# Kernel optimization log

Measured on AMD Instinct MI355X. Metric: run time of the kernel, lower is better.

## Reference

```python
import jax, jax.numpy as jnp
import numpy as np

WINDOW = 128
BACKWARD = 1
FORWARD = 0

def look_around(x, pad_value):
    # x: [b, windows, window_size, ...]; pad window axis and gather shifted windows
    w = x.shape[1]
    pads = [(0, 0), (BACKWARD, FORWARD)] + [(0, 0)] * (x.ndim - 2)
    p = jnp.pad(x, pads, constant_values=pad_value)
    return jnp.concatenate([p[:, i:i + w] for i in range(BACKWARD + FORWARD + 1)], axis=2)

def setup_inputs() -> dict:
    key = jax.random.key(0)
    ks = jax.random.split(key, 5)
    shp = (2, 16, 4096, 64)
    names = ['q', 'k', 'q_rot', 'k_rot', 'v']
    inp = {n: jax.random.normal(ks[i], shp, dtype=jnp.float32) for i, n in enumerate(names)}
    inp['states'] = 0
    inp['inferring_states'] = 0
    return inp

def reference(q, k, q_rot, k_rot, v, states, inferring_states):
    shape = q.shape
    merge = lambda t: t.reshape(-1, t.shape[-2], t.shape[-1])
    q, k, q_rot, k_rot, v = map(merge, (q, k, q_rot, k_rot, v))
    b, t, e = q.shape
    windows = t // WINDOW
    ticker = jnp.arange(t, dtype=q.dtype)[None, :]
    b_t = ticker.reshape(1, windows, WINDOW)
    bucket = lambda x: x.reshape(b, windows, WINDOW, e)
    bq, bk, bq_rot, bk_rot, bv = map(bucket, (q, k, q_rot, k_rot, v))
    bk = look_around(bk, 0.0)
    bk_rot = look_around(bk_rot, 0.0)
    bv = look_around(bv, 0.0)
    bq_t = b_t
    bq_k = look_around(b_t, -1.0)
    scale = e ** (-0.5)
    dots = jnp.einsum('bwie,bwje->bwij', bq, bk) * scale
    dots_rot = jnp.einsum('bwie,bwje->bwij', bq_rot, bk_rot) * scale
    mask_value = -jnp.finfo(dots.dtype).max
    causal_mask = bq_t[:, :, :, None] < bq_k[:, :, None, :]
    pad_mask = bq_k[:, :, None, :] == -1
    mask = causal_mask | pad_mask
    dots = jnp.where(mask, mask_value, dots)
    dots_rot = jnp.where(mask, mask_value, dots_rot)
    attn = jax.nn.softmax(dots + dots_rot, axis=-1)
    out = jnp.einsum('bwij,bwje->bwie', attn, bv)
    return out.reshape(shape)
```

## Files before the change

### kernel.cpp

```cpp
#include <hip/hip_runtime.h>
#include <stdint.h>

#define T 4096
#define E 64
#define NBH 32
#define W 4
#define LDK 136
#define CHUNK_KK (128*LDK)
#define CHUNK_VT (64*LDK)
#define BUF_ELEMS (CHUNK_KK + CHUNK_VT)
#define SMEM_BYTES (2*BUF_ELEMS*2)

typedef __attribute__((ext_vector_type(8))) short short8;
typedef __attribute__((ext_vector_type(4))) short short4v;
typedef __attribute__((ext_vector_type(4))) float f32x4;

__device__ __forceinline__ short f2bf(float x) {
  unsigned u = __float_as_uint(x);
  u += 0x7fffu + ((u >> 16) & 1u);
  return (short)(u >> 16);
}

struct ChunkStage { float4 sk[8]; float sv[16]; };

__device__ __forceinline__ void chunk_issue(ChunkStage& st,
    const float* __restrict__ k, const float* __restrict__ kr,
    const float* __restrict__ v, size_t rowbase, int tid, int wid, int lane) {
#pragma unroll
  for (int m = 0; m < 2; ++m) {
    const float* src = m ? kr : k;
#pragma unroll
    for (int it = 0; it < 4; ++it) {
      int idx = it * 512 + tid;
      st.sk[m * 4 + it] = *(const float4*)(src + (rowbase + (idx >> 4)) * E + (idx & 15) * 4);
    }
  }
  const float* vp = v + (rowbase + wid * 16) * E + lane;
#pragma unroll
  for (int i = 0; i < 16; ++i) st.sv[i] = vp[(size_t)i * E];
}

__device__ __forceinline__ void chunk_commit(const ChunkStage& st,
    short* __restrict__ KK, short* __restrict__ Vt, int tid, int wid, int lane) {
#pragma unroll
  for (int m = 0; m < 2; ++m) {
#pragma unroll
    for (int it = 0; it < 4; ++it) {
      int idx = it * 512 + tid;
      float4 f = st.sk[m * 4 + it];
      short4v h = { f2bf(f.x), f2bf(f.y), f2bf(f.z), f2bf(f.w) };
      *(short4v*)(KK + (idx >> 4) * LDK + m * 64 + (idx & 15) * 4) = h;
    }
  }
#pragma unroll
  for (int rq = 0; rq < 4; ++rq) {
    short4v h = { f2bf(st.sv[rq*4+0]), f2bf(st.sv[rq*4+1]),
                  f2bf(st.sv[rq*4+2]), f2bf(st.sv[rq*4+3]) };
    *(short4v*)(Vt + lane * LDK + wid * 16 + rq * 4) = h;
  }
}

__device__ __forceinline__ void q_issue(float4* sq,
    const float* __restrict__ q, const float* __restrict__ qr,
    size_t rbase, int w, int wid, int li, int lg) {
  const size_t qrow = rbase + (size_t)w * 128 + wid * 16 + li;
#pragma unroll
  for (int kt = 0; kt < 4; ++kt) {
    const float* sp = (kt < 2 ? q : qr) + qrow * E + (kt & 1) * 32 + lg * 8;
    sq[kt * 2 + 0] = *(const float4*)sp;
    sq[kt * 2 + 1] = *(const float4*)(sp + 4);
  }
}

__device__ __forceinline__ void q_commit(const float4* sq, short8* aF) {
#pragma unroll
  for (int kt = 0; kt < 4; ++kt) {
    float4 f0 = sq[kt * 2], f1 = sq[kt * 2 + 1];
    short8 a;
    a[0]=f2bf(f0.x*0.125f); a[1]=f2bf(f0.y*0.125f); a[2]=f2bf(f0.z*0.125f); a[3]=f2bf(f0.w*0.125f);
    a[4]=f2bf(f1.x*0.125f); a[5]=f2bf(f1.y*0.125f); a[6]=f2bf(f1.z*0.125f); a[7]=f2bf(f1.w*0.125f);
    aF[kt] = a;
  }
}

__global__ __launch_bounds__(512, 2)
void la_attn(const float* __restrict__ qg, const float* __restrict__ kg,
             const float* __restrict__ qrg, const float* __restrict__ krg,
             const float* __restrict__ vg, float* __restrict__ outg) {
  extern __shared__ short smem[];

  const int strip = blockIdx.x, bh = blockIdx.y;
  const int w0 = strip * W;
  const int tid = threadIdx.x;
  const int wid = tid >> 6, lane = tid & 63;
  const int li = lane & 15, lg = lane >> 4;
  const size_t rbase = (size_t)bh * T;
  const int rowb = wid * 16 + lg * 4;

  short8 aF[4];

  {
    ChunkStage s1, s0;
    float4 sq[8];
    if (w0 > 0) chunk_issue(s1, kg, krg, vg, rbase + (size_t)(w0 - 1) * 128, tid, wid, lane);
    chunk_issue(s0, kg, krg, vg, rbase + (size_t)w0 * 128, tid, wid, lane);
    q_issue(sq, qg, qrg, rbase, w0, wid, li, lg);
    if (w0 > 0) chunk_commit(s1, smem + BUF_ELEMS, smem + BUF_ELEMS + CHUNK_KK, tid, wid, lane);
    chunk_commit(s0, smem, smem + CHUNK_KK, tid, wid, lane);
    q_commit(sq, aF);
  }
  __syncthreads();

  for (int j = 0; j < W; ++j) {
    short* bufb = smem + ((j + 1) & 1) * BUF_ELEMS;
    short* bufc = smem + (j & 1) * BUF_ELEMS;
    short* KKback = bufb;       short* Vtback = bufb + CHUNK_KK;
    short* KKcur  = bufc;       short* Vtcur  = bufc + CHUNK_KK;
    const bool have_next = (j + 1 < W);
    const bool skipback = (w0 == 0 && j == 0);

    ChunkStage st;
    float4 sq[8];
    if (have_next) {
      chunk_issue(st, kg, krg, vg, rbase + (size_t)(w0 + j + 1) * 128, tid, wid, lane);
      q_issue(sq, qg, qrg, rbase, w0 + j + 1, wid, li, lg);
    }

    f32x4 S[16];
    if (!skipback) {
#pragma unroll
      for (int ct = 0; ct < 8; ++ct) {
        f32x4 acc = {0.f, 0.f, 0.f, 0.f};
        const short* kb = KKback + (ct * 16 + li) * LDK + lg * 8;
#pragma unroll
        for (int kt = 0; kt < 4; ++kt)
          acc = __builtin_amdgcn_mfma_f32_16x16x32_bf16(aF[kt], *(const short8*)(kb + kt * 32), acc, 0, 0, 0);
        S[ct] = acc;
      }
    } else {
#pragma unroll
      for (int ct = 0; ct < 8; ++ct) S[ct] = f32x4{-1e30f, -1e30f, -1e30f, -1e30f};
    }
#pragma unroll
    for (int ct = 0; ct < 8; ++ct) {
      f32x4 acc = {0.f, 0.f, 0.f, 0.f};
      const short* kb = KKcur + (ct * 16 + li) * LDK + lg * 8;
#pragma unroll
      for (int kt = 0; kt < 4; ++kt)
        acc = __builtin_amdgcn_mfma_f32_16x16x32_bf16(aF[kt], *(const short8*)(kb + kt * 32), acc, 0, 0, 0);
      S[8 + ct] = acc;
    }

    float linv[4];
#pragma unroll
    for (int r = 0; r < 4; ++r) {
      const int qi = rowb + r;
#pragma unroll
      for (int ct = 8; ct < 16; ++ct) {
        int jj = (ct - 8) * 16 + li;
        if (jj > qi) S[ct][r] = -1e30f;
      }
      float mx = -1e30f;
#pragma unroll
      for (int ct = 0; ct < 16; ++ct) mx = fmaxf(mx, S[ct][r]);
      mx = fmaxf(mx, __shfl_xor(mx, 1));
      mx = fmaxf(mx, __shfl_xor(mx, 2));
      mx = fmaxf(mx, __shfl_xor(mx, 4));
      mx = fmaxf(mx, __shfl_xor(mx, 8));
      float sm = 0.f;
#pragma unroll
      for (int ct = 0; ct < 16; ++ct) {
        float e = __expf(S[ct][r] - mx);
        S[ct][r] = e;
        sm += e;
      }
      sm += __shfl_xor(sm, 1);
      sm += __shfl_xor(sm, 2);
      sm += __shfl_xor(sm, 4);
      sm += __shfl_xor(sm, 8);
      linv[r] = 1.f / sm;
    }
    __syncthreads();

    short* pw = KKback + wid * 16 * LDK;
    f32x4 O[4] = {{0,0,0,0},{0,0,0,0},{0,0,0,0},{0,0,0,0}};
#pragma unroll
    for (int h = 0; h < 2; ++h) {
      if (h == 0 && skipback) continue;
      const short* Vth = h ? Vtcur : Vtback;
#pragma unroll
      for (int cc = 0; cc < 8; ++cc)
#pragma unroll
        for (int r = 0; r < 4; ++r)
          pw[(lg * 4 + r) * LDK + cc * 16 + li] = f2bf(S[h * 8 + cc][r]);
#pragma unroll
      for (int kt = 0; kt < 4; ++kt) {
        short8 aP = *(const short8*)(pw + li * LDK + kt * 32 + lg * 8);
#pragma unroll
        for (int nt = 0; nt < 4; ++nt) {
          short8 b = *(const short8*)(Vth + (nt * 16 + li) * LDK + kt * 32 + lg * 8);
          O[nt] = __builtin_amdgcn_mfma_f32_16x16x32_bf16(aP, b, O[nt], 0, 0, 0);
        }
      }
    }

    float* op = outg + (rbase + (size_t)(w0 + j) * 128 + rowb) * E;
#pragma unroll
    for (int r = 0; r < 4; ++r)
#pragma unroll
      for (int nt = 0; nt < 4; ++nt)
        op[(size_t)r * E + nt * 16 + li] = O[nt][r] * linv[r];

    __syncthreads();

    if (have_next) {
      chunk_commit(st, KKback, Vtback, tid, wid, lane);
      q_commit(sq, aF);
    }
    __syncthreads();
  }
}

extern "C" void kernel_launch(void* const* d_in, const int* in_sizes, int n_in,
                              void* d_out, int out_size, void* d_ws, size_t ws_size,
                              hipStream_t stream) {
  const float* q  = (const float*)d_in[0];
  const float* k  = (const float*)d_in[1];
  const float* qr = (const float*)d_in[2];
  const float* kr = (const float*)d_in[3];
  const float* v  = (const float*)d_in[4];
  float* out = (float*)d_out;
  la_attn<<<dim3(8, NBH), 512, SMEM_BYTES, stream>>>(q, k, qr, kr, v, out);
}
```

Measured before the change: 206.2 us.

## Split window softmax into online two-chunk pass and pipeline chunk loads two ahead

```diff
diff --git a/kernel.cpp b/kernel.cpp
--- a/kernel.cpp
+++ b/kernel.cpp
@@ -9,7 +9,8 @@
 #define CHUNK_KK (128*LDK)
 #define CHUNK_VT (64*LDK)
 #define BUF_ELEMS (CHUNK_KK + CHUNK_VT)
-#define SMEM_BYTES (2*BUF_ELEMS*2)
+#define PW_ELEMS (16*LDK)
+#define SMEM_BYTES ((2*BUF_ELEMS + 8*PW_ELEMS)*2)
 
 typedef __attribute__((ext_vector_type(8))) short short8;
 typedef __attribute__((ext_vector_type(4))) short short4v;
@@ -19,6 +20,12 @@
   unsigned u = __float_as_uint(x);
   u += 0x7fffu + ((u >> 16) & 1u);
   return (short)(u >> 16);
+}
+
+__device__ __forceinline__ void block_sync_lds() {
+  asm volatile("s_waitcnt lgkmcnt(0)" ::: "memory");
+  __builtin_amdgcn_s_barrier();
+  asm volatile("" ::: "memory");
 }
 
 struct ChunkStage { float4 sk[8]; float sv[16]; };
@@ -97,37 +104,40 @@
   const size_t rbase = (size_t)bh * T;
   const int rowb = wid * 16 + lg * 4;
 
+  short* PW = smem + 2 * BUF_ELEMS + wid * PW_ELEMS;
+  const int pxor_w = lg << 4;
+  const int pxor_r = (li >> 2) << 4;
+
   short8 aF[4];
+  ChunkStage st;
 
   {
-    ChunkStage s1, s0;
+    ChunkStage sm1, s0;
     float4 sq[8];
-    if (w0 > 0) chunk_issue(s1, kg, krg, vg, rbase + (size_t)(w0 - 1) * 128, tid, wid, lane);
+    if (w0 > 0) chunk_issue(sm1, kg, krg, vg, rbase + (size_t)(w0 - 1) * 128, tid, wid, lane);
     chunk_issue(s0, kg, krg, vg, rbase + (size_t)w0 * 128, tid, wid, lane);
     q_issue(sq, qg, qrg, rbase, w0, wid, li, lg);
-    if (w0 > 0) chunk_commit(s1, smem + BUF_ELEMS, smem + BUF_ELEMS + CHUNK_KK, tid, wid, lane);
+    if (w0 > 0) chunk_commit(sm1, smem + BUF_ELEMS, smem + BUF_ELEMS + CHUNK_KK, tid, wid, lane);
     chunk_commit(s0, smem, smem + CHUNK_KK, tid, wid, lane);
     q_commit(sq, aF);
-  }
-  __syncthreads();
+    chunk_issue(st, kg, krg, vg, rbase + (size_t)(w0 + 1) * 128, tid, wid, lane);
+  }
+  block_sync_lds();
 
   for (int j = 0; j < W; ++j) {
     short* bufb = smem + ((j + 1) & 1) * BUF_ELEMS;
     short* bufc = smem + (j & 1) * BUF_ELEMS;
     short* KKback = bufb;       short* Vtback = bufb + CHUNK_KK;
     short* KKcur  = bufc;       short* Vtcur  = bufc + CHUNK_KK;
-    const bool have_next = (j + 1 < W);
     const bool skipback = (w0 == 0 && j == 0);
 
-    ChunkStage st;
-    float4 sq[8];
-    if (have_next) {
-      chunk_issue(st, kg, krg, vg, rbase + (size_t)(w0 + j + 1) * 128, tid, wid, lane);
-      q_issue(sq, qg, qrg, rbase, w0 + j + 1, wid, li, lg);
-    }
-
-    f32x4 S[16];
+    float m[4], l[4];
+    f32x4 O[4] = {{0,0,0,0},{0,0,0,0},{0,0,0,0},{0,0,0,0}};
+#pragma unroll
+    for (int r = 0; r < 4; ++r) { m[r] = -1e30f; l[r] = 0.f; }
+
     if (!skipback) {
+      f32x4 S[8];
 #pragma unroll
       for (int ct = 0; ct < 8; ++ct) {
         f32x4 acc = {0.f, 0.f, 0.f, 0.f};
@@ -137,87 +147,124 @@
           acc = __builtin_amdgcn_mfma_f32_16x16x32_bf16(aF[kt], *(const short8*)(kb + kt * 32), acc, 0, 0, 0);
         S[ct] = acc;
       }
-    } else {
-#pragma unroll
-      for (int ct = 0; ct < 8; ++ct) S[ct] = f32x4{-1e30f, -1e30f, -1e30f, -1e30f};
-    }
-#pragma unroll
-    for (int ct = 0; ct < 8; ++ct) {
-      f32x4 acc = {0.f, 0.f, 0.f, 0.f};
-      const short* kb = KKcur + (ct * 16 + li) * LDK + lg * 8;
-#pragma unroll
-      for (int kt = 0; kt < 4; ++kt)
-        acc = __builtin_amdgcn_mfma_f32_16x16x32_bf16(aF[kt], *(const short8*)(kb + kt * 32), acc, 0, 0, 0);
-      S[8 + ct] = acc;
-    }
-
-    float linv[4];
+#pragma unroll
+      for (int r = 0; r < 4; ++r) {
+        float mx = S[0][r];
+#pragma unroll
+        for (int ct = 1; ct < 8; ++ct) mx = fmaxf(mx, S[ct][r]);
+        mx = fmaxf(mx, __shfl_xor(mx, 1));
+        mx = fmaxf(mx, __shfl_xor(mx, 2));
+        mx = fmaxf(mx, __shfl_xor(mx, 4));
+        mx = fmaxf(mx, __shfl_xor(mx, 8));
+        float sm = 0.f;
+#pragma unroll
+        for (int ct = 0; ct < 8; ++ct) {
+          float e = __expf(S[ct][r] - mx);
+          S[ct][r] = e;
+          sm += e;
+        }
+        sm += __shfl_xor(sm, 1);
+        sm += __shfl_xor(sm, 2);
+        sm += __shfl_xor(sm, 4);
+        sm += __shfl_xor(sm, 8);
+        m[r] = mx; l[r] = sm;
+      }
+#pragma unroll
+      for (int cc = 0; cc < 8; ++cc)
+#pragma unroll
+        for (int r = 0; r < 4; ++r)
+          PW[(lg * 4 + r) * LDK + ((cc * 16 + li) ^ pxor_w)] = f2bf(S[cc][r]);
+#pragma unroll
+      for (int kt = 0; kt < 4; ++kt) {
+        short8 aP = *(const short8*)(PW + li * LDK + ((kt * 32 + lg * 8) ^ pxor_r));
+#pragma unroll
+        for (int nt = 0; nt < 4; ++nt) {
+          short8 b = *(const short8*)(Vtback + (nt * 16 + li) * LDK + kt * 32 + lg * 8);
+          O[nt] = __builtin_amdgcn_mfma_f32_16x16x32_bf16(aP, b, O[nt], 0, 0, 0);
+        }
+      }
+    }
+
+    block_sync_lds();
+
+    const bool have_next = (j + 1 < W);
+    if (have_next) chunk_commit(st, KKback, Vtback, tid, wid, lane);
+    float4 sq[8];
+    if (j + 2 < W) chunk_issue(st, kg, krg, vg, rbase + (size_t)(w0 + j + 2) * 128, tid, wid, lane);
+    if (have_next) q_issue(sq, qg, qrg, rbase, w0 + j + 1, wid, li, lg);
+    asm volatile("" ::: "memory");
+
+    {
+      f32x4 S[8];
+#pragma unroll
+      for (int ct = 0; ct < 8; ++ct) {
+        f32x4 acc = {0.f, 0.f, 0.f, 0.f};
+        const short* kb = KKcur + (ct * 16 + li) * LDK + lg * 8;
+#pragma unroll
+        for (int kt = 0; kt < 4; ++kt)
+          acc = __builtin_amdgcn_mfma_f32_16x16x32_bf16(aF[kt], *(const short8*)(kb + kt * 32), acc, 0, 0, 0);
+        S[ct] = acc;
+      }
+#pragma unroll
+      for (int r = 0; r < 4; ++r) {
+        const int qi = rowb + r;
+#pragma unroll
+        for (int ct = 0; ct < 8; ++ct) {
+          int jj = ct * 16 + li;
+          if (jj > qi) S[ct][r] = -1e30f;
+        }
+        float mx = S[0][r];
+#pragma unroll
+        for (int ct = 1; ct < 8; ++ct) mx = fmaxf(mx, S[ct][r]);
+        mx = fmaxf(mx, __shfl_xor(mx, 1));
+        mx = fmaxf(mx, __shfl_xor(mx, 2));
+        mx = fmaxf(mx, __shfl_xor(mx, 4));
+        mx = fmaxf(mx, __shfl_xor(mx, 8));
+        float mn = fmaxf(m[r], mx);
+        float f = __expf(m[r] - mn);
+        float sm = 0.f;
+#pragma unroll
+        for (int ct = 0; ct < 8; ++ct) {
+          float e = __expf(S[ct][r] - mn);
+          S[ct][r] = e;
+          sm += e;
+        }
+        sm += __shfl_xor(sm, 1);
+        sm += __shfl_xor(sm, 2);
+        sm += __shfl_xor(sm, 4);
+        sm += __shfl_xor(sm, 8);
+        l[r] = l[r] * f + sm;
+        m[r] = mn;
+#pragma unroll
+        for (int nt = 0; nt < 4; ++nt) O[nt][r] *= f;
+      }
+#pragma unroll
+      for (int cc = 0; cc < 8; ++cc)
+#pragma unroll
+        for (int r = 0; r < 4; ++r)
+          PW[(lg * 4 + r) * LDK + ((cc * 16 + li) ^ pxor_w)] = f2bf(S[cc][r]);
+#pragma unroll
+      for (int kt = 0; kt < 4; ++kt) {
+        short8 aP = *(const short8*)(PW + li * LDK + ((kt * 32 + lg * 8) ^ pxor_r));
+#pragma unroll
+        for (int nt = 0; nt < 4; ++nt) {
+          short8 b = *(const short8*)(Vtcur + (nt * 16 + li) * LDK + kt * 32 + lg * 8);
+          O[nt] = __builtin_amdgcn_mfma_f32_16x16x32_bf16(aP, b, O[nt], 0, 0, 0);
+        }
+      }
+    }
+
+    float* op = outg + (rbase + (size_t)(w0 + j) * 128 + rowb) * E;
 #pragma unroll
     for (int r = 0; r < 4; ++r) {
-      const int qi = rowb + r;
-#pragma unroll
-      for (int ct = 8; ct < 16; ++ct) {
-        int jj = (ct - 8) * 16 + li;
-        if (jj > qi) S[ct][r] = -1e30f;
-      }
-      float mx = -1e30f;
-#pragma unroll
-      for (int ct = 0; ct < 16; ++ct) mx = fmaxf(mx, S[ct][r]);
-      mx = fmaxf(mx, __shfl_xor(mx, 1));
-      mx = fmaxf(mx, __shfl_xor(mx, 2));
-      mx = fmaxf(mx, __shfl_xor(mx, 4));
-      mx = fmaxf(mx, __shfl_xor(mx, 8));
-      float sm = 0.f;
-#pragma unroll
-      for (int ct = 0; ct < 16; ++ct) {
-        float e = __expf(S[ct][r] - mx);
-        S[ct][r] = e;
-        sm += e;
-      }
-      sm += __shfl_xor(sm, 1);
-      sm += __shfl_xor(sm, 2);
-      sm += __shfl_xor(sm, 4);
-      sm += __shfl_xor(sm, 8);
-      linv[r] = 1.f / sm;
-    }
-    __syncthreads();
-
-    short* pw = KKback + wid * 16 * LDK;
-    f32x4 O[4] = {{0,0,0,0},{0,0,0,0},{0,0,0,0},{0,0,0,0}};
-#pragma unroll
-    for (int h = 0; h < 2; ++h) {
-      if (h == 0 && skipback) continue;
-      const short* Vth = h ? Vtcur : Vtback;
-#pragma unroll
-      for (int cc = 0; cc < 8; ++cc)
-#pragma unroll
-        for (int r = 0; r < 4; ++r)
-          pw[(lg * 4 + r) * LDK + cc * 16 + li] = f2bf(S[h * 8 + cc][r]);
-#pragma unroll
-      for (int kt = 0; kt < 4; ++kt) {
-        short8 aP = *(const short8*)(pw + li * LDK + kt * 32 + lg * 8);
-#pragma unroll
-        for (int nt = 0; nt < 4; ++nt) {
-          short8 b = *(const short8*)(Vth + (nt * 16 + li) * LDK + kt * 32 + lg * 8);
-          O[nt] = __builtin_amdgcn_mfma_f32_16x16x32_bf16(aP, b, O[nt], 0, 0, 0);
-        }
-      }
-    }
-
-    float* op = outg + (rbase + (size_t)(w0 + j) * 128 + rowb) * E;
-#pragma unroll
-    for (int r = 0; r < 4; ++r)
+      float linv = 1.f / l[r];
 #pragma unroll
       for (int nt = 0; nt < 4; ++nt)
-        op[(size_t)r * E + nt * 16 + li] = O[nt][r] * linv[r];
-
-    __syncthreads();
-
-    if (have_next) {
-      chunk_commit(st, KKback, Vtback, tid, wid, lane);
-      q_commit(sq, aF);
-    }
-    __syncthreads();
+        op[(size_t)r * E + nt * 16 + li] = O[nt][r] * linv;
+    }
+
+    if (have_next) q_commit(sq, aF);
+    block_sync_lds();
   }
 }
 
```

Result: no change. 207.2 us (+0.5%).

## Launch one block per window with online softmax over 64-key sub-chunks

Applied to the files above, without the earlier changes.

```diff
diff --git a/kernel.cpp b/kernel.cpp
--- a/kernel.cpp
+++ b/kernel.cpp
@@ -4,12 +4,15 @@
 #define T 4096
 #define E 64
 #define NBH 32
-#define W 4
+#define NWIN 32
 #define LDK 136
-#define CHUNK_KK (128*LDK)
-#define CHUNK_VT (64*LDK)
-#define BUF_ELEMS (CHUNK_KK + CHUNK_VT)
-#define SMEM_BYTES (2*BUF_ELEMS*2)
+#define LDV 72
+#define LDP 72
+#define KK_ELEMS (64*LDK)
+#define VT_ELEMS (64*LDV)
+#define BUF_ELEMS (KK_ELEMS+VT_ELEMS)
+#define PW_ELEMS (16*LDP)
+#define SMEM_BYTES ((2*BUF_ELEMS + 8*PW_ELEMS)*2)
 
 typedef __attribute__((ext_vector_type(8))) short short8;
 typedef __attribute__((ext_vector_type(4))) short short4v;
@@ -21,42 +24,47 @@
   return (short)(u >> 16);
 }
 
-struct ChunkStage { float4 sk[8]; float sv[16]; };
-
-__device__ __forceinline__ void chunk_issue(ChunkStage& st,
+__device__ __forceinline__ void block_sync_lds() {
+  asm volatile("s_waitcnt lgkmcnt(0)" ::: "memory");
+  __builtin_amdgcn_s_barrier();
+  asm volatile("" ::: "memory");
+}
+
+struct SubStage { float4 sk[4]; float sv[8]; };
+
+__device__ __forceinline__ void sub_issue(SubStage& st,
     const float* __restrict__ k, const float* __restrict__ kr,
     const float* __restrict__ v, size_t rowbase, int tid, int wid, int lane) {
 #pragma unroll
   for (int m = 0; m < 2; ++m) {
     const float* src = m ? kr : k;
 #pragma unroll
-    for (int it = 0; it < 4; ++it) {
+    for (int it = 0; it < 2; ++it) {
       int idx = it * 512 + tid;
-      st.sk[m * 4 + it] = *(const float4*)(src + (rowbase + (idx >> 4)) * E + (idx & 15) * 4);
-    }
-  }
-  const float* vp = v + (rowbase + wid * 16) * E + lane;
-#pragma unroll
-  for (int i = 0; i < 16; ++i) st.sv[i] = vp[(size_t)i * E];
-}
-
-__device__ __forceinline__ void chunk_commit(const ChunkStage& st,
+      st.sk[m * 2 + it] = *(const float4*)(src + (rowbase + (idx >> 4)) * E + (idx & 15) * 4);
+    }
+  }
+  const float* vp = v + (rowbase + wid * 8) * E + lane;
+#pragma unroll
+  for (int i = 0; i < 8; ++i) st.sv[i] = vp[(size_t)i * E];
+}
+
+__device__ __forceinline__ void sub_commit(const SubStage& st,
     short* __restrict__ KK, short* __restrict__ Vt, int tid, int wid, int lane) {
 #pragma unroll
-  for (int m = 0; m < 2; ++m) {
-#pragma unroll
-    for (int it = 0; it < 4; ++it) {
+  for (int m = 0; m < 2; ++m)
+#pragma unroll
+    for (int it = 0; it < 2; ++it) {
       int idx = it * 512 + tid;
-      float4 f = st.sk[m * 4 + it];
+      float4 f = st.sk[m * 2 + it];
       short4v h = { f2bf(f.x), f2bf(f.y), f2bf(f.z), f2bf(f.w) };
       *(short4v*)(KK + (idx >> 4) * LDK + m * 64 + (idx & 15) * 4) = h;
     }
-  }
-#pragma unroll
-  for (int rq = 0; rq < 4; ++rq) {
+#pragma unroll
+  for (int rq = 0; rq < 2; ++rq) {
     short4v h = { f2bf(st.sv[rq*4+0]), f2bf(st.sv[rq*4+1]),
                   f2bf(st.sv[rq*4+2]), f2bf(st.sv[rq*4+3]) };
-    *(short4v*)(Vt + lane * LDK + wid * 16 + rq * 4) = h;
+    *(short4v*)(Vt + lane * LDV + wid * 8 + rq * 4) = h;
   }
 }
 
@@ -83,94 +91,93 @@
   }
 }
 
-__global__ __launch_bounds__(512, 2)
+__global__ __launch_bounds__(512, 4)
 void la_attn(const float* __restrict__ qg, const float* __restrict__ kg,
              const float* __restrict__ qrg, const float* __restrict__ krg,
              const float* __restrict__ vg, float* __restrict__ outg) {
   extern __shared__ short smem[];
 
-  const int strip = blockIdx.x, bh = blockIdx.y;
-  const int w0 = strip * W;
+  const int lid = blockIdx.y * NWIN + blockIdx.x;
+  const int wl  = (lid & 7) * 128 + (lid >> 3);
+  const int win = wl & (NWIN - 1), bh = wl >> 5;
+
   const int tid = threadIdx.x;
   const int wid = tid >> 6, lane = tid & 63;
   const int li = lane & 15, lg = lane >> 4;
   const size_t rbase = (size_t)bh * T;
   const int rowb = wid * 16 + lg * 4;
 
+  short* PW = smem + 2 * BUF_ELEMS + wid * PW_ELEMS;
+  const int pxor_w = lg << 4;
+  const int pxor_r = (li >> 2) << 4;
+
   short8 aF[4];
+  SubStage st;
+
+  const int s0 = (win == 0) ? 2 : 0;
+#define KROW(s) (rbase + (size_t)(win * 128 + ((s) - 2) * 64))
 
   {
-    ChunkStage s1, s0;
+    SubStage stA;
     float4 sq[8];
-    if (w0 > 0) chunk_issue(s1, kg, krg, vg, rbase + (size_t)(w0 - 1) * 128, tid, wid, lane);
-    chunk_issue(s0, kg, krg, vg, rbase + (size_t)w0 * 128, tid, wid, lane);
-    q_issue(sq, qg, qrg, rbase, w0, wid, li, lg);
-    if (w0 > 0) chunk_commit(s1, smem + BUF_ELEMS, smem + BUF_ELEMS + CHUNK_KK, tid, wid, lane);
-    chunk_commit(s0, smem, smem + CHUNK_KK, tid, wid, lane);
+    sub_issue(stA, kg, krg, vg, KROW(s0), tid, wid, lane);
+    q_issue(sq, qg, qrg, rbase, win, wid, li, lg);
+    sub_commit(stA, smem, smem + KK_ELEMS, tid, wid, lane);
     q_commit(sq, aF);
-  }
-  __syncthreads();
-
-  for (int j = 0; j < W; ++j) {
-    short* bufb = smem + ((j + 1) & 1) * BUF_ELEMS;
-    short* bufc = smem + (j & 1) * BUF_ELEMS;
-    short* KKback = bufb;       short* Vtback = bufb + CHUNK_KK;
-    short* KKcur  = bufc;       short* Vtcur  = bufc + CHUNK_KK;
-    const bool have_next = (j + 1 < W);
-    const bool skipback = (w0 == 0 && j == 0);
-
-    ChunkStage st;
-    float4 sq[8];
-    if (have_next) {
-      chunk_issue(st, kg, krg, vg, rbase + (size_t)(w0 + j + 1) * 128, tid, wid, lane);
-      q_issue(sq, qg, qrg, rbase, w0 + j + 1, wid, li, lg);
-    }
-
-    f32x4 S[16];
-    if (!skipback) {
-#pragma unroll
-      for (int ct = 0; ct < 8; ++ct) {
-        f32x4 acc = {0.f, 0.f, 0.f, 0.f};
-        const short* kb = KKback + (ct * 16 + li) * LDK + lg * 8;
-#pragma unroll
-        for (int kt = 0; kt < 4; ++kt)
-          acc = __builtin_amdgcn_mfma_f32_16x16x32_bf16(aF[kt], *(const short8*)(kb + kt * 32), acc, 0, 0, 0);
-        S[ct] = acc;
-      }
-    } else {
-#pragma unroll
-      for (int ct = 0; ct < 8; ++ct) S[ct] = f32x4{-1e30f, -1e30f, -1e30f, -1e30f};
-    }
-#pragma unroll
-    for (int ct = 0; ct < 8; ++ct) {
+    if (s0 + 1 < 4) sub_issue(st, kg, krg, vg, KROW(s0 + 1), tid, wid, lane);
+  }
+  block_sync_lds();
+
+  float m[4], l[4];
+  f32x4 O[4] = {{0,0,0,0},{0,0,0,0},{0,0,0,0},{0,0,0,0}};
+#pragma unroll
+  for (int r = 0; r < 4; ++r) { m[r] = -1e30f; l[r] = 0.f; }
+
+  for (int s = s0; s < 4; ++s) {
+    const int cur = (s - s0) & 1;
+    short* KKc = smem + cur * BUF_ELEMS;
+    short* Vtc = KKc + KK_ELEMS;
+
+    if (s + 1 < 4) {
+      sub_commit(st, smem + (cur ^ 1) * BUF_ELEMS,
+                 smem + (cur ^ 1) * BUF_ELEMS + KK_ELEMS, tid, wid, lane);
+      if (s + 2 < 4) sub_issue(st, kg, krg, vg, KROW(s + 2), tid, wid, lane);
+      asm volatile("" ::: "memory");
+    }
+
+    f32x4 S[4];
+#pragma unroll
+    for (int ct = 0; ct < 4; ++ct) {
       f32x4 acc = {0.f, 0.f, 0.f, 0.f};
-      const short* kb = KKcur + (ct * 16 + li) * LDK + lg * 8;
+      const short* kb = KKc + (ct * 16 + li) * LDK + lg * 8;
 #pragma unroll
       for (int kt = 0; kt < 4; ++kt)
         acc = __builtin_amdgcn_mfma_f32_16x16x32_bf16(aF[kt], *(const short8*)(kb + kt * 32), acc, 0, 0, 0);
-      S[8 + ct] = acc;
-    }
-
-    float linv[4];
+      S[ct] = acc;
+    }
+
+    const bool causal = (s >= 2);
 #pragma unroll
     for (int r = 0; r < 4; ++r) {
       const int qi = rowb + r;
-#pragma unroll
-      for (int ct = 8; ct < 16; ++ct) {
-        int jj = (ct - 8) * 16 + li;
-        if (jj > qi) S[ct][r] = -1e30f;
+      if (causal) {
+#pragma unroll
+        for (int ct = 0; ct < 4; ++ct) {
+          int jj = (s - 2) * 64 + ct * 16 + li;
+          if (jj > qi) S[ct][r] = -1e30f;
+        }
       }
-      float mx = -1e30f;
-#pragma unroll
-      for (int ct = 0; ct < 16; ++ct) mx = fmaxf(mx, S[ct][r]);
+      float mx = fmaxf(fmaxf(S[0][r], S[1][r]), fmaxf(S[2][r], S[3][r]));
       mx = fmaxf(mx, __shfl_xor(mx, 1));
       mx = fmaxf(mx, __shfl_xor(mx, 2));
       mx = fmaxf(mx, __shfl_xor(mx, 4));
       mx = fmaxf(mx, __shfl_xor(mx, 8));
+      float mn = fmaxf(m[r], mx);
+      float f = __expf(m[r] - mn);
       float sm = 0.f;
 #pragma unroll
-      for (int ct = 0; ct < 16; ++ct) {
-        float e = __expf(S[ct][r] - mx);
+      for (int ct = 0; ct < 4; ++ct) {
+        float e = __expf(S[ct][r] - mn);
         S[ct][r] = e;
         sm += e;
       }
@@ -178,47 +185,39 @@
       sm += __shfl_xor(sm, 2);
       sm += __shfl_xor(sm, 4);
       sm += __shfl_xor(sm, 8);
-      linv[r] = 1.f / sm;
-    }
-    __syncthreads();
-
-    short* pw = KKback + wid * 16 * LDK;
-    f32x4 O[4] = {{0,0,0,0},{0,0,0,0},{0,0,0,0},{0,0,0,0}};
-#pragma unroll
-    for (int h = 0; h < 2; ++h) {
-      if (h == 0 && skipback) continue;
-      const short* Vth = h ? Vtcur : Vtback;
-#pragma unroll
-      for (int cc = 0; cc < 8; ++cc)
-#pragma unroll
-        for (int r = 0; r < 4; ++r)
-          pw[(lg * 4 + r) * LDK + cc * 16 + li] = f2bf(S[h * 8 + cc][r]);
-#pragma unroll
-      for (int kt = 0; kt < 4; ++kt) {
-        short8 aP = *(const short8*)(pw + li * LDK + kt * 32 + lg * 8);
-#pragma unroll
-        for (int nt = 0; nt < 4; ++nt) {
-          short8 b = *(const short8*)(Vth + (nt * 16 + li) * LDK + kt * 32 + lg * 8);
-          O[nt] = __builtin_amdgcn_mfma_f32_16x16x32_bf16(aP, b, O[nt], 0, 0, 0);
-        }
+      l[r] = l[r] * f + sm;
+      m[r] = mn;
+#pragma unroll
+      for (int nt = 0; nt < 4; ++nt) O[nt][r] *= f;
+    }
+
+#pragma unroll
+    for (int cc = 0; cc < 4; ++cc)
+#pragma unroll
+      for (int r = 0; r < 4; ++r)
+        PW[(lg * 4 + r) * LDP + ((cc * 16 + li) ^ pxor_w)] = f2bf(S[cc][r]);
+#pragma unroll
+    for (int kt = 0; kt < 2; ++kt) {
+      short8 aP = *(const short8*)(PW + li * LDP + ((kt * 32 + lg * 8) ^ pxor_r));
+#pragma unroll
+      for (int nt = 0; nt < 4; ++nt) {
+        short8 b = *(const short8*)(Vtc + (nt * 16 + li) * LDV + kt * 32 + lg * 8);
+        O[nt] = __builtin_amdgcn_mfma_f32_16x16x32_bf16(aP, b, O[nt], 0, 0, 0);
       }
     }
 
-    float* op = outg + (rbase + (size_t)(w0 + j) * 128 + rowb) * E;
-#pragma unroll
-    for (int r = 0; r < 4; ++r)
-#pragma unroll
-      for (int nt = 0; nt < 4; ++nt)
-        op[(size_t)r * E + nt * 16 + li] = O[nt][r] * linv[r];
-
-    __syncthreads();
-
-    if (have_next) {
-      chunk_commit(st, KKback, Vtback, tid, wid, lane);
-      q_commit(sq, aF);
-    }
-    __syncthreads();
-  }
+    block_sync_lds();
+  }
+
+  float* op = outg + (rbase + (size_t)win * 128 + rowb) * E;
+#pragma unroll
+  for (int r = 0; r < 4; ++r) {
+    float linv = 1.f / l[r];
+#pragma unroll
+    for (int nt = 0; nt < 4; ++nt)
+      op[(size_t)r * E + nt * 16 + li] = O[nt][r] * linv;
+  }
+#undef KROW
 }
 
 extern "C" void kernel_launch(void* const* d_in, const int* in_sizes, int n_in,
@@ -230,5 +229,5 @@
   const float* kr = (const float*)d_in[3];
   const float* v  = (const float*)d_in[4];
   float* out = (float*)d_out;
-  la_attn<<<dim3(8, NBH), 512, SMEM_BYTES, stream>>>(q, k, qr, kr, v, out);
-}
+  la_attn<<<dim3(NWIN, NBH), 512, SMEM_BYTES, stream>>>(q, k, qr, kr, v, out);
+}
```

New measurement: 209.9 us. About the same (+1.8%).
